# Kernel optimization log

Hardware: AMD Instinct MI355X
Metric: run time of the kernel (lower is better)

The kernel has to match this reference:

```python
import jax, jax.numpy as jnp
import numpy as np

N_NODES = 50000
N_EDGES = 600000
D = 128
HIDDEN = 128
N_GRAPHS = 128
N_CLASSES = 10
N_STACKED = 3  # num_layers - 1


def setup_inputs() -> dict:
    key = jax.random.key(0)
    ks = jax.random.split(key, 12)
    s = 1.0 / np.sqrt(HIDDEN)
    inp = {
        "x": jax.random.normal(ks[0], (N_NODES, D), dtype=jnp.float32),
        "edge_index": jax.random.randint(ks[1], (2, N_EDGES), 0, N_NODES, dtype=jnp.int64),
        "batch": jnp.sort(jax.random.randint(ks[2], (N_NODES,), 0, N_GRAPHS, dtype=jnp.int64)),
        "W1": jax.random.normal(ks[3], (D, HIDDEN), dtype=jnp.float32) * s,
        "R1": jax.random.normal(ks[4], (D, HIDDEN), dtype=jnp.float32) * s,
        "b1": jnp.zeros((HIDDEN,), dtype=jnp.float32),
        "Wc": jax.random.normal(ks[5], (N_STACKED, HIDDEN, HIDDEN), dtype=jnp.float32) * s,
        "Rc": jax.random.normal(ks[6], (N_STACKED, HIDDEN, HIDDEN), dtype=jnp.float32) * s,
        "bc": jnp.zeros((N_STACKED, HIDDEN), dtype=jnp.float32),
        "lin1_w": jax.random.normal(ks[7], (HIDDEN, HIDDEN), dtype=jnp.float32) * s,
        "lin1_b": jnp.zeros((HIDDEN,), dtype=jnp.float32),
        "lin2_w": jax.random.normal(ks[8], (HIDDEN, N_CLASSES), dtype=jnp.float32) * s,
        "lin2_b": jnp.zeros((N_CLASSES,), dtype=jnp.float32),
    }
    return inp


def _gcn_norm(edge_index, n_nodes):
    # symmetric GCN normalization coeffs per edge (edge_weight=None -> ones)
    src, dst = edge_index[0], edge_index[1]
    ones = jnp.ones((edge_index.shape[1],), dtype=jnp.float32)
    deg = jax.ops.segment_sum(ones, dst, num_segments=n_nodes)
    dinv = jnp.where(deg > 0, jax.lax.rsqrt(jnp.maximum(deg, 1.0)), 0.0)
    return dinv[src] * dinv[dst]


def _gcs(x, src, dst, norm, W, R, b):
    # GCN aggregation on transformed features + linear skip (root) connection
    h = x @ W                                   # [N, H]
    msg = h[src] * norm[:, None]                # gather + scale, [E, H]
    agg = jax.ops.segment_sum(msg, dst, num_segments=x.shape[0])
    return agg + x @ R + b


def reference(x, edge_index, batch, W1, R1, b1, Wc, Rc, bc,
              lin1_w, lin1_b, lin2_w, lin2_b):
    src, dst = edge_index[0], edge_index[1]
    norm = _gcn_norm(edge_index, x.shape[0])

    h = jax.nn.relu(_gcs(x, src, dst, norm, W1, R1, b1))
    for i in range(N_STACKED):
        h = jax.nn.relu(_gcs(h, src, dst, norm, Wc[i], Rc[i], bc[i]))
    last = h

    # global mean pool over graphs
    sums = jax.ops.segment_sum(h, batch, num_segments=N_GRAPHS)
    cnts = jax.ops.segment_sum(jnp.ones((h.shape[0],), h.dtype), batch,
                               num_segments=N_GRAPHS)
    pooled = sums / jnp.maximum(cnts, 1.0)[:, None]

    g = jax.nn.relu(pooled @ lin1_w + lin1_b)   # dropout is identity in eval mode
    logits = g @ lin2_w + lin2_b
    return jax.nn.log_softmax(logits, axis=-1), last
```

## Files before the change

kernel.cpp:

```cpp
#include <hip/hip_runtime.h>

#define N_NODES  50000
#define N_EDGES  600000
#define DIM      128
#define N_GRAPHS 128
#define N_CLASSES 10
#define NB_SCAN  196
#define LDSW     136
#define ZWORDS   1700000
#define NZB4     1661


typedef __bf16 bf16x8 __attribute__((ext_vector_type(8)));
typedef float  f32x4  __attribute__((ext_vector_type(4)));

__device__ inline unsigned short f2bf(float f) {
  union { float f; unsigned int i; } u; u.f = f;
  unsigned int r = u.i + 0x7fff + ((u.i >> 16) & 1);
  return (unsigned short)(r >> 16);
}
__device__ inline float bf2f(unsigned short s) {
  union { unsigned int i; float f; } u; u.i = ((unsigned int)s) << 16;
  return u.f;
}
__device__ inline bf16x8 pack8(float4 lo, float4 hi) {
  union { bf16x8 v; unsigned short s[8]; } u;
  u.s[0] = f2bf(lo.x); u.s[1] = f2bf(lo.y); u.s[2] = f2bf(lo.z); u.s[3] = f2bf(lo.w);
  u.s[4] = f2bf(hi.x); u.s[5] = f2bf(hi.y); u.s[6] = f2bf(hi.z); u.s[7] = f2bf(hi.w);
  return u.v;
}


__global__ __launch_bounds__(256) void k_prep(float4* __restrict__ z4,
                                              const float* __restrict__ W1,
                                              const float* __restrict__ R1,
                                              const float* __restrict__ Wc,
                                              const float* __restrict__ Rc,
                                              unsigned short* __restrict__ pk) {
  if (blockIdx.x < NZB4) {
    int i = blockIdx.x * 256 + threadIdx.x;
    if (i < ZWORDS / 4) z4[i] = make_float4(0.f, 0.f, 0.f, 0.f);
    return;
  }
  int pb = blockIdx.x - NZB4;
  int mm = pb >> 3, sub = pb & 7;
  const float* src = (mm == 0) ? W1
                   : (mm < 4)  ? Wc + (size_t)(mm - 1) * DIM * DIM
                   : (mm == 4) ? R1
                               : Rc + (size_t)(mm - 5) * DIM * DIM;
  int idx = sub * 256 + threadIdx.x;
  int lane = idx & 63;
  int kc   = (idx >> 6) & 3;
  int nt   = idx >> 8;
  int col  = nt * 16 + (lane & 15);
  int k0   = kc * 32 + (lane >> 4) * 8;
  unsigned short* dst = pk + (size_t)mm * 16384 + (size_t)idx * 8;
  ushort4 u;
  u.x = f2bf(src[(k0 + 0) * DIM + col]);
  u.y = f2bf(src[(k0 + 1) * DIM + col]);
  u.z = f2bf(src[(k0 + 2) * DIM + col]);
  u.w = f2bf(src[(k0 + 3) * DIM + col]);
  *(ushort4*)&dst[0] = u;
  u.x = f2bf(src[(k0 + 4) * DIM + col]);
  u.y = f2bf(src[(k0 + 5) * DIM + col]);
  u.z = f2bf(src[(k0 + 6) * DIM + col]);
  u.w = f2bf(src[(k0 + 7) * DIM + col]);
  *(ushort4*)&dst[4] = u;
}


__global__ __launch_bounds__(256) void k_deg(const int* __restrict__ ei,
                                             int* __restrict__ deg) {
  int e = blockIdx.x * 256 + threadIdx.x;
  if (e < N_EDGES) atomicAdd(&deg[ei[N_EDGES + e]], 1);
}

__global__ __launch_bounds__(256) void k_dinvsum(const int* __restrict__ deg,
                                                 float* __restrict__ dinv,
                                                 int* __restrict__ bsum) {
  int i = blockIdx.x * 256 + threadIdx.x;
  int t = threadIdx.x;
  int d = (i < N_NODES) ? deg[i] : 0;
  if (i < N_NODES) dinv[i] = (d > 0) ? rsqrtf((float)d) : 0.f;
  int dp = (d + 3) & ~3;
  __shared__ int tmp[256];
  tmp[t] = dp;
  __syncthreads();
  for (int off = 128; off > 0; off >>= 1) {
    if (t < off) tmp[t] += tmp[t + off];
    __syncthreads();
  }
  if (t == 0) bsum[blockIdx.x] = tmp[0];
}

__global__ __launch_bounds__(256) void k_bscan(const int* __restrict__ bsum,
                                               int* __restrict__ boff,
                                               int* __restrict__ rowp) {
  int t = threadIdx.x;
  int v = (t < NB_SCAN) ? bsum[t] : 0;
  __shared__ int tmp[256];
  tmp[t] = v;
  __syncthreads();
  for (int off = 1; off < 256; off <<= 1) {
    int add = (t >= off) ? tmp[t - off] : 0;
    __syncthreads();
    tmp[t] += add;
    __syncthreads();
  }
  boff[t] = tmp[t] - v;
  if (t == 255) rowp[N_NODES] = tmp[255];
}

__global__ __launch_bounds__(256) void k_rowp(const int* __restrict__ deg,
                                              const int* __restrict__ boff,
                                              int* __restrict__ rowp) {
  int i = blockIdx.x * 256 + threadIdx.x;
  int t = threadIdx.x;
  int dp = (i < N_NODES) ? ((deg[i] + 3) & ~3) : 0;
  __shared__ int tmp[256];
  tmp[t] = dp;
  __syncthreads();
  for (int off = 1; off < 256; off <<= 1) {
    int add = (t >= off) ? tmp[t - off] : 0;
    __syncthreads();
    tmp[t] += add;
    __syncthreads();
  }
  if (i < N_NODES) rowp[i] = boff[blockIdx.x] + tmp[t] - dp;
}

__global__ __launch_bounds__(256) void k_fill(const int* __restrict__ ei,
                                              const int* __restrict__ rowp,
                                              int* __restrict__ cnt,
                                              const float* __restrict__ dinv,
                                              int2* __restrict__ epk) {
  int e = blockIdx.x * 256 + threadIdx.x;
  if (e < N_EDGES) {
    int s = ei[e];
    int d = ei[N_EDGES + e];
    int p = rowp[d] + atomicAdd(&cnt[d], 1);
    epk[p] = make_int2(s, __float_as_int(dinv[s] * dinv[d]));
  }
}


__global__ __launch_bounds__(256) void k_gemm0(const float* __restrict__ xf,
                                               const unsigned short* __restrict__ pkW,
                                               const unsigned short* __restrict__ pkR,
                                               const float* __restrict__ bv,
                                               unsigned short* __restrict__ hwb,
                                               unsigned short* __restrict__ skipb) {
  const int tid  = threadIdx.x;
  const int wave = tid >> 6, lane = tid & 63;
  const int m = lane & 15, q = lane >> 4;
  const int rbase = blockIdx.x * 64 + wave * 16;
  const int arow  = rbase + m;
  const bool aok  = arow < N_NODES;

  bf16x8 a[4];
#pragma unroll
  for (int kc = 0; kc < 4; ++kc) {
    float4 lo = make_float4(0.f, 0.f, 0.f, 0.f);
    float4 hi = make_float4(0.f, 0.f, 0.f, 0.f);
    if (aok) {
      lo = *(const float4*)&xf[arow * DIM + kc * 32 + q * 8];
      hi = *(const float4*)&xf[arow * DIM + kc * 32 + q * 8 + 4];
    }
    a[kc] = pack8(lo, hi);
  }

  f32x4 acc[16];
#pragma unroll
  for (int t = 0; t < 16; ++t) acc[t] = (f32x4){0.f, 0.f, 0.f, 0.f};

#pragma unroll
  for (int nt = 0; nt < 8; ++nt) {
    const unsigned short* pw = pkW + ((size_t)(nt * 4) * 64 + lane) * 8;
    const unsigned short* pr = pkR + ((size_t)(nt * 4) * 64 + lane) * 8;
#pragma unroll
    for (int kc = 0; kc < 4; ++kc) {
      bf16x8 bW = *(const bf16x8*)(pw + (size_t)kc * 64 * 8);
      acc[nt] = __builtin_amdgcn_mfma_f32_16x16x32_bf16(a[kc], bW, acc[nt], 0, 0, 0);
    }
#pragma unroll
    for (int kc = 0; kc < 4; ++kc) {
      bf16x8 bR = *(const bf16x8*)(pr + (size_t)kc * 64 * 8);
      acc[8 + nt] = __builtin_amdgcn_mfma_f32_16x16x32_bf16(a[kc], bR, acc[8 + nt], 0, 0, 0);
    }
  }

#pragma unroll
  for (int nt = 0; nt < 8; ++nt) {
    int col = nt * 16 + m;
    float bias = bv[col];
#pragma unroll
    for (int rg = 0; rg < 4; ++rg) {
      int row = rbase + q * 4 + rg;
      if (row < N_NODES) {
        hwb[row * DIM + col]   = f2bf(acc[nt][rg]);
        skipb[row * DIM + col] = f2bf(acc[8 + nt][rg] + bias);
      }
    }
  }
}


template<bool LAST>
__global__ __launch_bounds__(256) void k_aggemm(const unsigned short* __restrict__ hin,
                                                const int* __restrict__ rowp,
                                                const int2* __restrict__ epk,
                                                const unsigned short* __restrict__ pkW,
                                                const unsigned short* __restrict__ pkR,
                                                const float* __restrict__ bv,
                                                unsigned short* __restrict__ hout,
                                                unsigned short* __restrict__ skipb,
                                                float* __restrict__ skipf) {
  __shared__ unsigned short xs[64 * LDSW];
  const int tid = threadIdx.x;
  const int row0 = blockIdx.x * 64;
  const int wave = tid >> 6, lane = tid & 63;

  {
    int h  = (tid >> 5) & 1;
    int l4 = (tid & 31) * 4;
    for (int rnd = 0; rnd < 8; ++rnd) {
      int r = wave * 16 + rnd * 2 + h;
      int n = row0 + r;
      float4 acc = make_float4(0.f, 0.f, 0.f, 0.f);
      if (n < N_NODES) {
        int e0 = rowp[n], e1 = rowp[n + 1];
        for (int e = e0; e < e1; e += 4) {
          int4 p0 = *(const int4*)&epk[e];
          int4 p1 = *(const int4*)&epk[e + 2];
          ushort4 u0 = *(const ushort4*)&hin[p0.x * DIM + l4];
          ushort4 u1 = *(const ushort4*)&hin[p0.z * DIM + l4];
          ushort4 u2 = *(const ushort4*)&hin[p1.x * DIM + l4];
          ushort4 u3 = *(const ushort4*)&hin[p1.z * DIM + l4];
          float w0 = __int_as_float(p0.y), w1 = __int_as_float(p0.w);
          float w2 = __int_as_float(p1.y), w3 = __int_as_float(p1.w);
          acc.x = fmaf(w0, bf2f(u0.x), fmaf(w1, bf2f(u1.x), fmaf(w2, bf2f(u2.x), fmaf(w3, bf2f(u3.x), acc.x))));
          acc.y = fmaf(w0, bf2f(u0.y), fmaf(w1, bf2f(u1.y), fmaf(w2, bf2f(u2.y), fmaf(w3, bf2f(u3.y), acc.y))));
          acc.z = fmaf(w0, bf2f(u0.z), fmaf(w1, bf2f(u1.z), fmaf(w2, bf2f(u2.z), fmaf(w3, bf2f(u3.z), acc.z))));
          acc.w = fmaf(w0, bf2f(u0.w), fmaf(w1, bf2f(u1.w), fmaf(w2, bf2f(u2.w), fmaf(w3, bf2f(u3.w), acc.w))));
        }
        ushort4 s = *(const ushort4*)&skipb[n * DIM + l4];
        acc.x = fmaxf(acc.x + bf2f(s.x), 0.f);
        acc.y = fmaxf(acc.y + bf2f(s.y), 0.f);
        acc.z = fmaxf(acc.z + bf2f(s.z), 0.f);
        acc.w = fmaxf(acc.w + bf2f(s.w), 0.f);
      }
      ushort4 o;
      o.x = f2bf(acc.x); o.y = f2bf(acc.y); o.z = f2bf(acc.z); o.w = f2bf(acc.w);
      *(ushort4*)&xs[r * LDSW + l4] = o;
    }
  }

  const int m = lane & 15, q = lane >> 4;
  const int rbase = row0 + wave * 16;

  bf16x8 a[4];
#pragma unroll
  for (int kc = 0; kc < 4; ++kc)
    a[kc] = *(const bf16x8*)&xs[(wave * 16 + m) * LDSW + kc * 32 + q * 8];

  f32x4 acc[16];
#pragma unroll
  for (int t = 0; t < 16; ++t) acc[t] = (f32x4){0.f, 0.f, 0.f, 0.f};

#pragma unroll
  for (int nt = 0; nt < 8; ++nt) {
    const unsigned short* pw = pkW + ((size_t)(nt * 4) * 64 + lane) * 8;
    const unsigned short* pr = pkR + ((size_t)(nt * 4) * 64 + lane) * 8;
#pragma unroll
    for (int kc = 0; kc < 4; ++kc) {
      bf16x8 bW = *(const bf16x8*)(pw + (size_t)kc * 64 * 8);
      acc[nt] = __builtin_amdgcn_mfma_f32_16x16x32_bf16(a[kc], bW, acc[nt], 0, 0, 0);
    }
#pragma unroll
    for (int kc = 0; kc < 4; ++kc) {
      bf16x8 bR = *(const bf16x8*)(pr + (size_t)kc * 64 * 8);
      acc[8 + nt] = __builtin_amdgcn_mfma_f32_16x16x32_bf16(a[kc], bR, acc[8 + nt], 0, 0, 0);
    }
  }

#pragma unroll
  for (int nt = 0; nt < 8; ++nt) {
    int col = nt * 16 + m;
    float bias = bv[col];
#pragma unroll
    for (int rg = 0; rg < 4; ++rg) {
      int row = rbase + q * 4 + rg;
      if (row < N_NODES) {
        hout[row * DIM + col] = f2bf(acc[nt][rg]);
        float v = acc[8 + nt][rg] + bias;
        if (LAST) skipf[row * DIM + col] = v;
        else      skipb[row * DIM + col] = f2bf(v);
      }
    }
  }
}


__global__ __launch_bounds__(256) void k_aggF(const unsigned short* __restrict__ hwb,
                                              const int* __restrict__ rowp,
                                              const int2* __restrict__ epk,
                                              float* __restrict__ actf) {
  int n = blockIdx.x * 8 + (threadIdx.x >> 5);
  if (n >= N_NODES) return;
  int l4 = (threadIdx.x & 31) * 4;
  float4 acc = make_float4(0.f, 0.f, 0.f, 0.f);
  int e0 = rowp[n], e1 = rowp[n + 1];
  for (int e = e0; e < e1; e += 4) {
    int4 p0 = *(const int4*)&epk[e];
    int4 p1 = *(const int4*)&epk[e + 2];
    ushort4 u0 = *(const ushort4*)&hwb[p0.x * DIM + l4];
    ushort4 u1 = *(const ushort4*)&hwb[p0.z * DIM + l4];
    ushort4 u2 = *(const ushort4*)&hwb[p1.x * DIM + l4];
    ushort4 u3 = *(const ushort4*)&hwb[p1.z * DIM + l4];
    float w0 = __int_as_float(p0.y), w1 = __int_as_float(p0.w);
    float w2 = __int_as_float(p1.y), w3 = __int_as_float(p1.w);
    acc.x = fmaf(w0, bf2f(u0.x), fmaf(w1, bf2f(u1.x), fmaf(w2, bf2f(u2.x), fmaf(w3, bf2f(u3.x), acc.x))));
    acc.y = fmaf(w0, bf2f(u0.y), fmaf(w1, bf2f(u1.y), fmaf(w2, bf2f(u2.y), fmaf(w3, bf2f(u3.y), acc.y))));
    acc.z = fmaf(w0, bf2f(u0.z), fmaf(w1, bf2f(u1.z), fmaf(w2, bf2f(u2.z), fmaf(w3, bf2f(u3.z), acc.z))));
    acc.w = fmaf(w0, bf2f(u0.w), fmaf(w1, bf2f(u1.w), fmaf(w2, bf2f(u2.w), fmaf(w3, bf2f(u3.w), acc.w))));
  }
  float4 s = *(const float4*)&actf[n * DIM + l4];
  acc.x = fmaxf(acc.x + s.x, 0.f);
  acc.y = fmaxf(acc.y + s.y, 0.f);
  acc.z = fmaxf(acc.z + s.z, 0.f);
  acc.w = fmaxf(acc.w + s.w, 0.f);
  *(float4*)&actf[n * DIM + l4] = acc;
}


__global__ __launch_bounds__(1024) void k_pool2(const float* __restrict__ h,
                                                const int* __restrict__ batch,
                                                float* __restrict__ pooled) {
  int g = blockIdx.x;
  int t = threadIdx.x;
  __shared__ int sb[2];
  if (t < 2) {
    int target = g + t;
    int lo = 0, hi = N_NODES;
    while (lo < hi) {
      int mid = (lo + hi) >> 1;
      if (batch[mid] < target) lo = mid + 1; else hi = mid;
    }
    sb[t] = lo;
  }
  __syncthreads();
  int start = sb[0], end = sb[1];
  int c = t & 127, rg = t >> 7;
  float acc = 0.f;
  for (int r = start + rg; r < end; r += 8) acc += h[r * DIM + c];
  __shared__ float sp[8][DIM];
  sp[rg][c] = acc;
  __syncthreads();
  if (rg == 0) {
    float tot = acc;
#pragma unroll
    for (int i = 1; i < 8; ++i) tot += sp[i][c];
    float cnt = fmaxf((float)(end - start), 1.f);
    pooled[g * DIM + c] = tot / cnt;
  }
}


__global__ __launch_bounds__(128) void k_mlp1(const float* __restrict__ pooled,
                                              const float* __restrict__ w,
                                              const float* __restrict__ bias,
                                              float* __restrict__ g1) {
  int g = blockIdx.x, t = threadIdx.x;
  __shared__ float sp[DIM];
  sp[t] = pooled[g * DIM + t];
  __syncthreads();
  float acc = bias[t];
#pragma unroll 4
  for (int k = 0; k < DIM; ++k) acc = fmaf(sp[k], w[k * DIM + t], acc);
  g1[g * DIM + t] = fmaxf(acc, 0.f);
}

__global__ __launch_bounds__(128) void k_mlp2(const float* __restrict__ g1,
                                              const float* __restrict__ w,
                                              const float* __restrict__ bias,
                                              float* __restrict__ out) {
  int g = threadIdx.x;
  float l[N_CLASSES];
#pragma unroll
  for (int c = 0; c < N_CLASSES; ++c) l[c] = bias[c];
  for (int k = 0; k < DIM; ++k) {
    float gv = g1[g * DIM + k];
#pragma unroll
    for (int c = 0; c < N_CLASSES; ++c) l[c] = fmaf(gv, w[k * N_CLASSES + c], l[c]);
  }
  float m = l[0];
#pragma unroll
  for (int c = 1; c < N_CLASSES; ++c) m = fmaxf(m, l[c]);
  float s = 0.f;
#pragma unroll
  for (int c = 0; c < N_CLASSES; ++c) s += expf(l[c] - m);
  float lse = logf(s) + m;
#pragma unroll
  for (int c = 0; c < N_CLASSES; ++c) out[g * N_CLASSES + c] = l[c] - lse;
}


extern "C" void kernel_launch(void* const* d_in, const int* in_sizes, int n_in,
                              void* d_out, int out_size, void* d_ws, size_t ws_size,
                              hipStream_t stream) {
  const float* x     = (const float*)d_in[0];
  const int* ei      = (const int*)d_in[1];
  const int* batch   = (const int*)d_in[2];
  const float* W1  = (const float*)d_in[3];
  const float* R1  = (const float*)d_in[4];
  const float* b1  = (const float*)d_in[5];
  const float* Wc  = (const float*)d_in[6];
  const float* Rc  = (const float*)d_in[7];
  const float* bc  = (const float*)d_in[8];
  const float* l1w = (const float*)d_in[9];
  const float* l1b = (const float*)d_in[10];
  const float* l2w = (const float*)d_in[11];
  const float* l2b = (const float*)d_in[12];

  float* out   = (float*)d_out;
  float* dlast = out + N_GRAPHS * N_CLASSES;

  float* ws = (float*)d_ws;
  unsigned short* h0    = (unsigned short*)ws;
  unsigned short* h1    = (unsigned short*)(ws + 3203072);
  unsigned short* skipb = (unsigned short*)(ws + 6406144);
  int*   deg   = (int*)(ws + 9609216);
  int*   cnt   = (int*)(ws + 9659216);
  int2*  epk   = (int2*)(ws + 9709216);
  float* dinv  = ws + 11309216;
  int*   rowp  = (int*)(ws + 11359216);
  float* pooled= ws + 11409232;
  float* g1    = ws + 11425616;
  unsigned short* pk = (unsigned short*)(ws + 11442000);
  int*   bsum  = (int*)(ws + 11507536);
  int*   boff  = (int*)(ws + 11507792);

  k_prep<<<NZB4 + 64, 256, 0, stream>>>((float4*)(ws + 9609216), W1, R1, Wc, Rc, pk);
  k_deg <<<(N_EDGES + 255) / 256, 256, 0, stream>>>(ei, deg);
  k_dinvsum<<<NB_SCAN, 256, 0, stream>>>(deg, dinv, bsum);
  k_bscan<<<1, 256, 0, stream>>>(bsum, boff, rowp);
  k_rowp<<<NB_SCAN, 256, 0, stream>>>(deg, boff, rowp);
  k_fill<<<(N_EDGES + 255) / 256, 256, 0, stream>>>(ei, rowp, cnt, dinv, epk);

  const int NGB = (N_NODES + 63) / 64;
  const int NAB = (N_NODES + 7) / 8;

  k_gemm0<<<NGB, 256, 0, stream>>>(x, pk + 0 * 16384, pk + 4 * 16384, b1, h0, skipb);
  k_aggemm<false><<<NGB, 256, 0, stream>>>(h0, rowp, epk,
      pk + 1 * 16384, pk + 5 * 16384, bc + 0 * DIM, h1, skipb, nullptr);
  k_aggemm<false><<<NGB, 256, 0, stream>>>(h1, rowp, epk,
      pk + 2 * 16384, pk + 6 * 16384, bc + 1 * DIM, h0, skipb, nullptr);
  k_aggemm<true><<<NGB, 256, 0, stream>>>(h0, rowp, epk,
      pk + 3 * 16384, pk + 7 * 16384, bc + 2 * DIM, h1, skipb, dlast);
  k_aggF<<<NAB, 256, 0, stream>>>(h1, rowp, epk, dlast);

  k_pool2<<<N_GRAPHS, 1024, 0, stream>>>(dlast, batch, pooled);
  k_mlp1<<<N_GRAPHS, 128, 0, stream>>>(pooled, l1w, l1b, g1);
  k_mlp2<<<1, N_GRAPHS, 0, stream>>>(g1, l2w, l2b, out);
}
```

Baseline: 398.8 us.

## Split fused gather+GEMM into separate gather and in-place GEMM kernels

Splits each fused aggregation+GEMM layer into two kernels: a gather kernel that writes the aggregated, skip-added, ReLU'd activations to global memory, and a GEMM kernel that reads them and writes its output in place. The aim is to let the irregular gather run at its own finer grid (8 nodes per block) and free the GEMM from LDS staging and load imbalance. The cost is an extra bf16 round-trip of the full node-feature matrix through global memory per layer, plus three more kernel launches.

```diff
diff --git a/kernel.cpp b/kernel.cpp
--- a/kernel.cpp
+++ b/kernel.cpp
@@ -6,7 +6,6 @@
 #define N_GRAPHS 128
 #define N_CLASSES 10
 #define NB_SCAN  196
-#define LDSW     136
 #define ZWORDS   1700000
 #define NZB4     1661
 
@@ -27,6 +26,12 @@
   union { bf16x8 v; unsigned short s[8]; } u;
   u.s[0] = f2bf(lo.x); u.s[1] = f2bf(lo.y); u.s[2] = f2bf(lo.z); u.s[3] = f2bf(lo.w);
   u.s[4] = f2bf(hi.x); u.s[5] = f2bf(hi.y); u.s[6] = f2bf(hi.z); u.s[7] = f2bf(hi.w);
+  return u.v;
+}
+__device__ inline bf16x8 zero8() {
+  union { bf16x8 v; unsigned short s[8]; } u;
+#pragma unroll
+  for (int j = 0; j < 8; ++j) u.s[j] = 0;
   return u.v;
 }
 
@@ -205,63 +210,58 @@
 }
 
 
+__global__ __launch_bounds__(256) void k_gath(const unsigned short* __restrict__ hin,
+                                              const int* __restrict__ rowp,
+                                              const int2* __restrict__ epk,
+                                              const unsigned short* __restrict__ skipb,
+                                              unsigned short* __restrict__ gout) {
+  int n = blockIdx.x * 8 + (threadIdx.x >> 5);
+  if (n >= N_NODES) return;
+  int l4 = (threadIdx.x & 31) * 4;
+  float4 acc = make_float4(0.f, 0.f, 0.f, 0.f);
+  int e0 = rowp[n], e1 = rowp[n + 1];
+  for (int e = e0; e < e1; e += 4) {
+    int4 p0 = *(const int4*)&epk[e];
+    int4 p1 = *(const int4*)&epk[e + 2];
+    ushort4 u0 = *(const ushort4*)&hin[p0.x * DIM + l4];
+    ushort4 u1 = *(const ushort4*)&hin[p0.z * DIM + l4];
+    ushort4 u2 = *(const ushort4*)&hin[p1.x * DIM + l4];
+    ushort4 u3 = *(const ushort4*)&hin[p1.z * DIM + l4];
+    float w0 = __int_as_float(p0.y), w1 = __int_as_float(p0.w);
+    float w2 = __int_as_float(p1.y), w3 = __int_as_float(p1.w);
+    acc.x = fmaf(w0, bf2f(u0.x), fmaf(w1, bf2f(u1.x), fmaf(w2, bf2f(u2.x), fmaf(w3, bf2f(u3.x), acc.x))));
+    acc.y = fmaf(w0, bf2f(u0.y), fmaf(w1, bf2f(u1.y), fmaf(w2, bf2f(u2.y), fmaf(w3, bf2f(u3.y), acc.y))));
+    acc.z = fmaf(w0, bf2f(u0.z), fmaf(w1, bf2f(u1.z), fmaf(w2, bf2f(u2.z), fmaf(w3, bf2f(u3.z), acc.z))));
+    acc.w = fmaf(w0, bf2f(u0.w), fmaf(w1, bf2f(u1.w), fmaf(w2, bf2f(u2.w), fmaf(w3, bf2f(u3.w), acc.w))));
+  }
+  ushort4 s = *(const ushort4*)&skipb[n * DIM + l4];
+  ushort4 o;
+  o.x = f2bf(fmaxf(acc.x + bf2f(s.x), 0.f));
+  o.y = f2bf(fmaxf(acc.y + bf2f(s.y), 0.f));
+  o.z = f2bf(fmaxf(acc.z + bf2f(s.z), 0.f));
+  o.w = f2bf(fmaxf(acc.w + bf2f(s.w), 0.f));
+  *(ushort4*)&gout[n * DIM + l4] = o;
+}
+
+
 template<bool LAST>
-__global__ __launch_bounds__(256) void k_aggemm(const unsigned short* __restrict__ hin,
-                                                const int* __restrict__ rowp,
-                                                const int2* __restrict__ epk,
-                                                const unsigned short* __restrict__ pkW,
-                                                const unsigned short* __restrict__ pkR,
-                                                const float* __restrict__ bv,
-                                                unsigned short* __restrict__ hout,
-                                                unsigned short* __restrict__ skipb,
-                                                float* __restrict__ skipf) {
-  __shared__ unsigned short xs[64 * LDSW];
-  const int tid = threadIdx.x;
-  const int row0 = blockIdx.x * 64;
+__global__ __launch_bounds__(256) void k_gemmb(unsigned short* __restrict__ gio,
+                                               const unsigned short* __restrict__ pkW,
+                                               const unsigned short* __restrict__ pkR,
+                                               const float* __restrict__ bv,
+                                               unsigned short* __restrict__ skipb,
+                                               float* __restrict__ skipf) {
+  const int tid  = threadIdx.x;
   const int wave = tid >> 6, lane = tid & 63;
-
-  {
-    int h  = (tid >> 5) & 1;
-    int l4 = (tid & 31) * 4;
-    for (int rnd = 0; rnd < 8; ++rnd) {
-      int r = wave * 16 + rnd * 2 + h;
-      int n = row0 + r;
-      float4 acc = make_float4(0.f, 0.f, 0.f, 0.f);
-      if (n < N_NODES) {
-        int e0 = rowp[n], e1 = rowp[n + 1];
-        for (int e = e0; e < e1; e += 4) {
-          int4 p0 = *(const int4*)&epk[e];
-          int4 p1 = *(const int4*)&epk[e + 2];
-          ushort4 u0 = *(const ushort4*)&hin[p0.x * DIM + l4];
-          ushort4 u1 = *(const ushort4*)&hin[p0.z * DIM + l4];
-          ushort4 u2 = *(const ushort4*)&hin[p1.x * DIM + l4];
-          ushort4 u3 = *(const ushort4*)&hin[p1.z * DIM + l4];
-          float w0 = __int_as_float(p0.y), w1 = __int_as_float(p0.w);
-          float w2 = __int_as_float(p1.y), w3 = __int_as_float(p1.w);
-          acc.x = fmaf(w0, bf2f(u0.x), fmaf(w1, bf2f(u1.x), fmaf(w2, bf2f(u2.x), fmaf(w3, bf2f(u3.x), acc.x))));
-          acc.y = fmaf(w0, bf2f(u0.y), fmaf(w1, bf2f(u1.y), fmaf(w2, bf2f(u2.y), fmaf(w3, bf2f(u3.y), acc.y))));
-          acc.z = fmaf(w0, bf2f(u0.z), fmaf(w1, bf2f(u1.z), fmaf(w2, bf2f(u2.z), fmaf(w3, bf2f(u3.z), acc.z))));
-          acc.w = fmaf(w0, bf2f(u0.w), fmaf(w1, bf2f(u1.w), fmaf(w2, bf2f(u2.w), fmaf(w3, bf2f(u3.w), acc.w))));
-        }
-        ushort4 s = *(const ushort4*)&skipb[n * DIM + l4];
-        acc.x = fmaxf(acc.x + bf2f(s.x), 0.f);
-        acc.y = fmaxf(acc.y + bf2f(s.y), 0.f);
-        acc.z = fmaxf(acc.z + bf2f(s.z), 0.f);
-        acc.w = fmaxf(acc.w + bf2f(s.w), 0.f);
-      }
-      ushort4 o;
-      o.x = f2bf(acc.x); o.y = f2bf(acc.y); o.z = f2bf(acc.z); o.w = f2bf(acc.w);
-      *(ushort4*)&xs[r * LDSW + l4] = o;
-    }
-  }
-
   const int m = lane & 15, q = lane >> 4;
-  const int rbase = row0 + wave * 16;
+  const int rbase = blockIdx.x * 64 + wave * 16;
+  const int arow  = rbase + m;
+  const bool aok  = arow < N_NODES;
 
   bf16x8 a[4];
 #pragma unroll
   for (int kc = 0; kc < 4; ++kc)
-    a[kc] = *(const bf16x8*)&xs[(wave * 16 + m) * LDSW + kc * 32 + q * 8];
+    a[kc] = aok ? *(const bf16x8*)&gio[arow * DIM + kc * 32 + q * 8] : zero8();
 
   f32x4 acc[16];
 #pragma unroll
@@ -291,7 +291,7 @@
     for (int rg = 0; rg < 4; ++rg) {
       int row = rbase + q * 4 + rg;
       if (row < N_NODES) {
-        hout[row * DIM + col] = f2bf(acc[nt][rg]);
+        gio[row * DIM + col] = f2bf(acc[nt][rg]);
         float v = acc[8 + nt][rg] + bias;
         if (LAST) skipf[row * DIM + col] = v;
         else      skipb[row * DIM + col] = f2bf(v);
@@ -426,9 +426,9 @@
   float* dlast = out + N_GRAPHS * N_CLASSES;
 
   float* ws = (float*)d_ws;
-  unsigned short* h0    = (unsigned short*)ws;
-  unsigned short* h1    = (unsigned short*)(ws + 3203072);
-  unsigned short* skipb = (unsigned short*)(ws + 6406144);
+  unsigned short* X = (unsigned short*)ws;
+  unsigned short* Y = (unsigned short*)(ws + 3203072);
+  unsigned short* S = (unsigned short*)(ws + 6406144);
   int*   deg   = (int*)(ws + 9609216);
   int*   cnt   = (int*)(ws + 9659216);
   int2*  epk   = (int2*)(ws + 9709216);
@@ -450,14 +450,17 @@
   const int NGB = (N_NODES + 63) / 64;
   const int NAB = (N_NODES + 7) / 8;
 
-  k_gemm0<<<NGB, 256, 0, stream>>>(x, pk + 0 * 16384, pk + 4 * 16384, b1, h0, skipb);
-  k_aggemm<false><<<NGB, 256, 0, stream>>>(h0, rowp, epk,
-      pk + 1 * 16384, pk + 5 * 16384, bc + 0 * DIM, h1, skipb, nullptr);
-  k_aggemm<false><<<NGB, 256, 0, stream>>>(h1, rowp, epk,
-      pk + 2 * 16384, pk + 6 * 16384, bc + 1 * DIM, h0, skipb, nullptr);
-  k_aggemm<true><<<NGB, 256, 0, stream>>>(h0, rowp, epk,
-      pk + 3 * 16384, pk + 7 * 16384, bc + 2 * DIM, h1, skipb, dlast);
-  k_aggF<<<NAB, 256, 0, stream>>>(h1, rowp, epk, dlast);
+  k_gemm0<<<NGB, 256, 0, stream>>>(x, pk + 0 * 16384, pk + 4 * 16384, b1, X, S);
+  k_gath <<<NAB, 256, 0, stream>>>(X, rowp, epk, S, Y);
+  k_gemmb<false><<<NGB, 256, 0, stream>>>(Y, pk + 1 * 16384, pk + 5 * 16384,
+                                          bc + 0 * DIM, S, nullptr);
+  k_gath <<<NAB, 256, 0, stream>>>(Y, rowp, epk, S, X);
+  k_gemmb<false><<<NGB, 256, 0, stream>>>(X, pk + 2 * 16384, pk + 6 * 16384,
+                                          bc + 1 * DIM, S, nullptr);
+  k_gath <<<NAB, 256, 0, stream>>>(X, rowp, epk, S, Y);
+  k_gemmb<true><<<NGB, 256, 0, stream>>>(Y, pk + 3 * 16384, pk + 7 * 16384,
+                                         bc + 2 * DIM, S, dlast);
+  k_aggF<<<NAB, 256, 0, stream>>>(Y, rowp, epk, dlast);
 
   k_pool2<<<N_GRAPHS, 1024, 0, stream>>>(dlast, batch, pooled);
   k_mlp1<<<N_GRAPHS, 128, 0, stream>>>(pooled, l1w, l1b, g1);
```

Result: faster. 387.5 us (-2.8%).
